# Kernel tuning notes

Hardware: AMD Instinct MI355X
Metric: run time of the kernel (lower is better)

## Reference

```python
import jax, jax.numpy as jnp
import numpy as np
import math

NUM_CLASSES = 91
FOCAL_ALPHA = 0.25
FOCAL_GAMMA = 2.0
BBOX_COEF = 5.0
GIOU_COEF = 2.0
ANGLE_COEF = 1.0
PI = math.pi


def _rect_corners(box):
    # box: [5] = (cx, cy, w, h, theta) -> [4,2] corners, CCW order
    cx, cy, w, h, th = box[0], box[1], box[2], box[3], box[4]
    c, s = jnp.cos(th), jnp.sin(th)
    dx = jnp.array([0.5, -0.5, -0.5, 0.5], box.dtype) * w
    dy = jnp.array([0.5, 0.5, -0.5, -0.5], box.dtype) * h
    px = cx + c * dx - s * dy
    py = cy + s * dx + c * dy
    return jnp.stack([px, py], axis=-1)


def _pair_obb_iou(b1, b2):
    # Oriented-box IoU of one pair via Sutherland-Hodgman convex clipping.
    # Intersection of two convex quads has at most 8 vertices.
    P = _rect_corners(b1)  # subject polygon [4,2]
    Q = _rect_corners(b2)  # clip polygon   [4,2]
    verts = jnp.concatenate([P, jnp.tile(P[:1], (4, 1))], axis=0)  # [8,2] padded
    n = jnp.int32(4)
    cQ = Q.mean(0)
    idx = jnp.arange(8)
    for k in range(4):  # clip against each edge of Q
        a, b = Q[k], Q[(k + 1) % 4]
        ex, ey = b[0] - a[0], b[1] - a[1]
        sd = lambda p: ex * (p[..., 1] - a[1]) - ey * (p[..., 0] - a[0])
        sgn = jnp.where(sd(cQ) >= 0, 1.0, -1.0)
        d = sd(verts) * sgn  # signed distance, >=0 means inside [8]
        nidx = jnp.where(idx == n - 1, 0, idx + 1)
        d_cur, d_nxt = d, d[nidx]
        valid_edge = idx < n
        cur_in, nxt_in = d_cur >= 0, d_nxt >= 0
        denom = d_cur - d_nxt
        t = jnp.where(jnp.abs(denom) > 1e-12, d_cur / jnp.where(denom == 0, 1.0, denom), 0.0)
        inter_pt = verts + t[:, None] * (verts[nidx] - verts)
        out_pts = jnp.zeros((16, 2), verts.dtype)
        out_pts = out_pts.at[0::2].set(inter_pt)
        out_pts = out_pts.at[1::2].set(verts[nidx])
        out_valid = jnp.zeros(16, bool)
        out_valid = out_valid.at[0::2].set(valid_edge & (cur_in != nxt_in))
        out_valid = out_valid.at[1::2].set(valid_edge & nxt_in)
        order = jnp.argsort(~out_valid)  # stable: valid points first, order kept
        verts = out_pts[order][:8]
        n = jnp.minimum(jnp.sum(out_valid), 8).astype(jnp.int32)
    # shoelace area; pad invalid slots with v0 so extra edges contribute 0
    verts = jnp.where((idx < n)[:, None], verts, verts[0][None])
    x, y = verts[:, 0], verts[:, 1]
    inter = 0.5 * jnp.abs(jnp.sum(x * jnp.roll(y, -1) - jnp.roll(x, -1) * y))
    a1 = b1[2] * b1[3]
    a2 = b2[2] * b2[3]
    union = a1 + a2 - inter
    return jnp.where(union > 0, inter / union, 0.0)


def _losses(pred_logits, pred_boxes, tgt_boxes, batch_idx, src_idx, tgt_labels, nb):
    B, Q, C = pred_logits.shape
    # ---- loss_labels: scatter one-hot + sigmoid focal loss ----
    target_classes = jnp.full((B, Q), NUM_CLASSES, jnp.int32)
    target_classes = target_classes.at[batch_idx, src_idx].set(tgt_labels.astype(jnp.int32))
    onehot = jax.nn.one_hot(target_classes, C + 1, dtype=pred_logits.dtype)[..., :C]
    prob = jax.nn.sigmoid(pred_logits)
    ce = jnp.maximum(pred_logits, 0) - pred_logits * onehot + jnp.log1p(jnp.exp(-jnp.abs(pred_logits)))
    p_t = prob * onehot + (1 - prob) * (1 - onehot)
    alpha_t = FOCAL_ALPHA * onehot + (1 - FOCAL_ALPHA) * (1 - onehot)
    focal = alpha_t * ce * (1 - p_t) ** FOCAL_GAMMA
    loss_ce = focal.mean(1).sum() / nb * Q
    # ---- loss_boxes: L1 + angle + oriented IoU ----
    src_boxes = pred_boxes[batch_idx, src_idx]  # [N,5]
    loss_bbox = jnp.abs(src_boxes[:, :4] - tgt_boxes[:, :4]).sum() / nb * BBOX_COEF
    ap, at = src_boxes[:, 4], tgt_boxes[:, 4]
    loss_angle = jnp.minimum(jnp.abs(ap - at), jnp.abs(ap - (at + PI))).sum() / nb * ANGLE_COEF
    iou = jax.vmap(_pair_obb_iou)(src_boxes, tgt_boxes)  # diag of obb_iou(src, tgt)
    loss_giou = (1.0 - iou).sum() / nb * GIOU_COEF
    return jnp.stack([loss_ce, loss_bbox, loss_giou, loss_angle])


def setup_inputs() -> dict:
    key = jax.random.key(0)
    ks = jax.random.split(key, 8)
    B, Q, C, N = 128, 900, 91, 8192
    pred_logits = jax.random.normal(ks[0], (B, Q, C), jnp.float32)
    def make_boxes(k, shape):
        k1, k2, k3 = jax.random.split(k, 3)
        xy = jax.random.uniform(k1, shape[:-1] + (2,), jnp.float32)
        wh = jax.random.uniform(k2, shape[:-1] + (2,), jnp.float32) * 0.2 + 0.05
        th = jax.random.uniform(k3, shape[:-1] + (1,), jnp.float32) * PI
        return jnp.concatenate([xy, wh, th], axis=-1)
    pred_boxes = make_boxes(ks[1], (B, Q, 5))
    tgt_boxes = make_boxes(ks[2], (N, 5))
    batch_idx = jnp.sort(jax.random.randint(ks[3], (N,), 0, B))
    src_idx = jax.random.randint(ks[4], (N,), 0, Q)
    tgt_labels = jax.random.randint(ks[5], (N,), 0, C)
    return {"pred_logits": pred_logits, "pred_boxes": pred_boxes, "tgt_boxes": tgt_boxes,
            "batch_idx": batch_idx, "src_idx": src_idx, "tgt_labels": tgt_labels, "num_boxes": N}


def reference(pred_logits, pred_boxes, tgt_boxes, batch_idx, src_idx, tgt_labels, num_boxes):
    nb = jnp.asarray(num_boxes, jnp.float32)
    return _losses(pred_logits, pred_boxes, tgt_boxes, batch_idx, src_idx, tgt_labels, nb)
```

## Files before the change

kernel.cpp:

```cpp
#include <hip/hip_runtime.h>
#include <math.h>

#define QN 900
#define CN 91
#define BQ (128 * 900)
#define NPAIR 8192
#define PI_F 3.14159265358979323846f

#define PAIR_BLOCKS 32
#define CORR_BLOCKS 450
#define FOCAL_BLOCKS 2048
#define NFLOAT4 (BQ * CN / 4)


__device__ __forceinline__ float read_nb(const void* p) {
    int iv = *(const int*)p;
    if (iv > 0 && iv < (1 << 30)) return (float)iv;
    return *(const float*)p;
}

__device__ __forceinline__ float f0_raw(float x) {
    float e   = __expf(-fabsf(x));
    float ope = 1.0f + e;
    float r   = __builtin_amdgcn_rcpf(ope);
    float l   = __logf(ope);
    float sp  = fmaxf(x, 0.0f) + l;
    float s   = (x >= 0.0f) ? r : e * r;
    return sp * s * s;
}


__global__ __launch_bounds__(256) void scatter_kernel(const int* __restrict__ bi,
                                                      const int* __restrict__ si,
                                                      const int* __restrict__ lb,
                                                      int* __restrict__ tc) {
    int i = blockIdx.x * 256 + threadIdx.x;
    if (i < NPAIR) {
        int key = (i << 7) | lb[i];
        atomicMax(&tc[bi[i] * QN + si[i]], key);
    }
}


__device__ void focal_body(int rb, const float4* __restrict__ l4, const void* nbp,
                           float* out, float* sm) {
    float acc = 0.0f;
    const int stride = FOCAL_BLOCKS * 256;
    for (int i = rb * 256 + threadIdx.x; i < NFLOAT4; i += stride) {
        float4 v = l4[i];
        acc += f0_raw(v.x);
        acc += f0_raw(v.y);
        acc += f0_raw(v.z);
        acc += f0_raw(v.w);
    }
#pragma unroll
    for (int o = 32; o > 0; o >>= 1) acc += __shfl_down(acc, o, 64);
    int lane = threadIdx.x & 63, w = threadIdx.x >> 6;
    if (lane == 0) sm[w] = acc;
    __syncthreads();
    if (threadIdx.x == 0) {
        float nb = read_nb(nbp);
        atomicAdd(out + 0, (sm[0] + sm[1] + sm[2] + sm[3]) * 0.75f / nb);
    }
}

__device__ void corr_body(int rb, const float* __restrict__ logits,
                          const int* __restrict__ tc, const void* nbp,
                          float* out, float* sm) {
    int j = rb * 256 + threadIdx.x;
    float acc = 0.0f;
    int v = tc[j];
    if (v >= 0) {
        int label = v & 127;
        float x = logits[j * CN + label];
        float e   = __expf(-fabsf(x));
        float ope = 1.0f + e;
        float r   = __builtin_amdgcn_rcpf(ope);
        float l   = __logf(ope);
        float sp_p = fmaxf(x, 0.0f) + l;
        float sp_n = fmaxf(-x, 0.0f) + l;
        float s   = (x >= 0.0f) ? r : e * r;
        float oms = 1.0f - s;
        acc = 0.25f * sp_n * oms * oms - 0.75f * sp_p * s * s;
    }
#pragma unroll
    for (int o = 32; o > 0; o >>= 1) acc += __shfl_down(acc, o, 64);
    int lane = threadIdx.x & 63, w = threadIdx.x >> 6;
    if (lane == 0) sm[w] = acc;
    __syncthreads();
    if (threadIdx.x == 0) {
        float nb = read_nb(nbp);
        atomicAdd(out + 0, (sm[0] + sm[1] + sm[2] + sm[3]) / nb);
    }
}

__device__ void pairs_body(const float* __restrict__ pb, const float* __restrict__ tb,
                           const int* __restrict__ bi, const int* __restrict__ si,
                           const void* nbp, float* out, float* sm) {
    int i = blockIdx.x * 256 + threadIdx.x;
    int b = bi[i], s = si[i];
    const float* p = pb + (b * QN + s) * 5;
    const float* t = tb + i * 5;
    float p0 = p[0], p1 = p[1], p2 = p[2], p3 = p[3], p4 = p[4];
    float t0 = t[0], t1 = t[1], t2 = t[2], t3 = t[3], t4 = t[4];

    float lb = fabsf(p0 - t0) + fabsf(p1 - t1) + fabsf(p2 - t2) + fabsf(p3 - t3);
    float la = fminf(fabsf(p4 - t4), fabsf(p4 - (t4 + PI_F)));

    const float dxs[4] = {0.5f, -0.5f, -0.5f, 0.5f};
    const float dys[4] = {0.5f, 0.5f, -0.5f, -0.5f};
    float c1 = cosf(p4), s1 = sinf(p4);
    float c2 = cosf(t4), s2 = sinf(t4);
    float px[8], py[8], qx[4], qy[4];
#pragma unroll
    for (int k = 0; k < 4; k++) {
        float dx = dxs[k] * p2, dy = dys[k] * p3;
        px[k] = p0 + c1 * dx - s1 * dy;
        py[k] = p1 + s1 * dx + c1 * dy;
        float ex = dxs[k] * t2, ey = dys[k] * t3;
        qx[k] = t0 + c2 * ex - s2 * ey;
        qy[k] = t1 + s2 * ex + c2 * ey;
    }
#pragma unroll
    for (int k = 4; k < 8; k++) { px[k] = 0.0f; py[k] = 0.0f; }
    float cqx = (qx[0] + qx[1] + qx[2] + qx[3]) * 0.25f;
    float cqy = (qy[0] + qy[1] + qy[2] + qy[3]) * 0.25f;

    int n = 4;
#pragma unroll
    for (int k = 0; k < 4; k++) {
        float ax = qx[k], ay = qy[k];
        int k2 = (k + 1) & 3;
        float ex = qx[k2] - ax, ey = qy[k2] - ay;
        float sd_c = ex * (cqy - ay) - ey * (cqx - ax);
        float sgn = (sd_c >= 0.0f) ? 1.0f : -1.0f;
        float d[8];
#pragma unroll
        for (int ii = 0; ii < 8; ii++)
            d[ii] = sgn * (ex * (py[ii] - ay) - ey * (px[ii] - ax));
        float nx[8], ny[8];
#pragma unroll
        for (int ii = 0; ii < 8; ii++) { nx[ii] = 0.0f; ny[ii] = 0.0f; }
        int m = 0;
#pragma unroll
        for (int ii = 0; ii < 8; ii++) {
            bool act  = ii < n;
            bool last = (ii == n - 1);
            float jx = last ? px[0] : (ii < 7 ? px[ii + 1] : 0.0f);
            float jy = last ? py[0] : (ii < 7 ? py[ii + 1] : 0.0f);
            float dn = last ? d[0]  : (ii < 7 ? d[ii + 1]  : 0.0f);
            float dc = d[ii];
            bool ci = dc >= 0.0f, ni_ = dn >= 0.0f;
            bool emitI = act && (ci != ni_);
            bool emitV = act && ni_;
            float den = dc - dn;
            float tt = (fabsf(den) > 1e-12f) ? (dc / den) : 0.0f;
            float ix = px[ii] + tt * (jx - px[ii]);
            float iy = py[ii] + tt * (jy - py[ii]);
#pragma unroll
            for (int ss = 0; ss < 8; ss++) {
                bool w1 = emitI && (ss == m);
                nx[ss] = w1 ? ix : nx[ss];
                ny[ss] = w1 ? iy : ny[ss];
            }
            m += emitI ? 1 : 0;
#pragma unroll
            for (int ss = 0; ss < 8; ss++) {
                bool w2 = emitV && (ss == m);
                nx[ss] = w2 ? jx : nx[ss];
                ny[ss] = w2 ? jy : ny[ss];
            }
            m += emitV ? 1 : 0;
        }
#pragma unroll
        for (int ii = 0; ii < 8; ii++) { px[ii] = nx[ii]; py[ii] = ny[ii]; }
        n = (m > 8) ? 8 : m;
    }
    float a2 = 0.0f;
#pragma unroll
    for (int ii = 0; ii < 8; ii++) {
        bool act  = ii < n;
        bool last = (ii == n - 1);
        float jx = last ? px[0] : (ii < 7 ? px[ii + 1] : 0.0f);
        float jy = last ? py[0] : (ii < 7 ? py[ii + 1] : 0.0f);
        a2 += act ? (px[ii] * jy - jx * py[ii]) : 0.0f;
    }
    float inter = 0.5f * fabsf(a2);
    float area1 = p2 * p3, area2 = t2 * t3;
    float uni = area1 + area2 - inter;
    float iou = (uni > 0.0f) ? inter / uni : 0.0f;
    float lg = 1.0f - iou;

#pragma unroll
    for (int o = 32; o > 0; o >>= 1) {
        lb += __shfl_down(lb, o, 64);
        lg += __shfl_down(lg, o, 64);
        la += __shfl_down(la, o, 64);
    }
    int lane = threadIdx.x & 63, w = threadIdx.x >> 6;
    if (lane == 0) { sm[w] = lb; sm[4 + w] = lg; sm[8 + w] = la; }
    __syncthreads();
    if (threadIdx.x == 0) {
        float nb = read_nb(nbp);
        float inv = 1.0f / nb;
        atomicAdd(out + 1, (sm[0] + sm[1] + sm[2] + sm[3]) * 5.0f * inv);
        atomicAdd(out + 2, (sm[4] + sm[5] + sm[6] + sm[7]) * 2.0f * inv);
        atomicAdd(out + 3, (sm[8] + sm[9] + sm[10] + sm[11]) * inv);
    }
}


__global__ __launch_bounds__(256) void mega_kernel(const float* __restrict__ logits,
                                                   const float* __restrict__ pboxes,
                                                   const float* __restrict__ tboxes,
                                                   const int* __restrict__ bidx,
                                                   const int* __restrict__ sidx,
                                                   const int* __restrict__ tc,
                                                   const void* __restrict__ nbp,
                                                   float* __restrict__ out) {
    __shared__ float sm[12];
    int rb = blockIdx.x;
    if (rb < PAIR_BLOCKS) {
        pairs_body(pboxes, tboxes, bidx, sidx, nbp, out, sm);
        return;
    }
    rb -= PAIR_BLOCKS;
    if (rb < CORR_BLOCKS) {
        corr_body(rb, logits, tc, nbp, out, sm);
        return;
    }
    rb -= CORR_BLOCKS;
    focal_body(rb, (const float4*)logits, nbp, out, sm);
}


extern "C" void kernel_launch(void* const* d_in, const int* in_sizes, int n_in,
                              void* d_out, int out_size, void* d_ws, size_t ws_size,
                              hipStream_t stream) {
    const float* logits = (const float*)d_in[0];
    const float* pboxes = (const float*)d_in[1];
    const float* tboxes = (const float*)d_in[2];
    const int*   bidx   = (const int*)d_in[3];
    const int*   sidx   = (const int*)d_in[4];
    const int*   labels = (const int*)d_in[5];
    const void*  nbp    = d_in[6];
    float* out = (float*)d_out;
    int*   tc  = (int*)d_ws;

    hipMemsetAsync(tc, 0xFF, BQ * sizeof(int), stream);
    hipMemsetAsync(out, 0, 4 * sizeof(float), stream);

    scatter_kernel<<<(NPAIR + 255) / 256, 256, 0, stream>>>(bidx, sidx, labels, tc);
    mega_kernel<<<PAIR_BLOCKS + CORR_BLOCKS + FOCAL_BLOCKS, 256, 0, stream>>>(
        logits, pboxes, tboxes, bidx, sidx, tc, nbp, out);
}
```

Baseline: 122.8 us.

## Fold matched-class correction into pairs kernel and split focal into own kernel

Instead of scanning all 115200 query slots to apply the matched-class correction, each of the 8192 pairs checks whether it won the atomicMax scatter for its slot and applies the correction itself, inside the pairs kernel. The single mega kernel is split into a standalone focal kernel and a combined pairs+correction kernel, launched in sequence. This drops 450 correction blocks but adds an extra kernel launch, and the pairs work now runs serially after the focal pass rather than overlapping with it.

```diff
diff --git a/kernel.cpp b/kernel.cpp
--- a/kernel.cpp
+++ b/kernel.cpp
@@ -7,8 +7,6 @@
 #define NPAIR 8192
 #define PI_F 3.14159265358979323846f
 
-#define PAIR_BLOCKS 32
-#define CORR_BLOCKS 450
 #define FOCAL_BLOCKS 2048
 #define NFLOAT4 (BQ * CN / 4)
 
@@ -35,18 +33,18 @@
                                                       const int* __restrict__ lb,
                                                       int* __restrict__ tc) {
     int i = blockIdx.x * 256 + threadIdx.x;
-    if (i < NPAIR) {
-        int key = (i << 7) | lb[i];
-        atomicMax(&tc[bi[i] * QN + si[i]], key);
-    }
-}
-
-
-__device__ void focal_body(int rb, const float4* __restrict__ l4, const void* nbp,
-                           float* out, float* sm) {
+    int key = (i << 7) | lb[i];
+    atomicMax(&tc[bi[i] * QN + si[i]], key);
+}
+
+
+__global__ __launch_bounds__(256) void focal_kernel(const float4* __restrict__ l4,
+                                                    const void* __restrict__ nbp,
+                                                    float* __restrict__ out) {
+    __shared__ float sm[4];
     float acc = 0.0f;
     const int stride = FOCAL_BLOCKS * 256;
-    for (int i = rb * 256 + threadIdx.x; i < NFLOAT4; i += stride) {
+    for (int i = blockIdx.x * 256 + threadIdx.x; i < NFLOAT4; i += stride) {
         float4 v = l4[i];
         acc += f0_raw(v.x);
         acc += f0_raw(v.y);
@@ -64,42 +62,37 @@
     }
 }
 
-__device__ void corr_body(int rb, const float* __restrict__ logits,
-                          const int* __restrict__ tc, const void* nbp,
-                          float* out, float* sm) {
-    int j = rb * 256 + threadIdx.x;
-    float acc = 0.0f;
-    int v = tc[j];
-    if (v >= 0) {
-        int label = v & 127;
-        float x = logits[j * CN + label];
+
+__global__ __launch_bounds__(256) void pairs_kernel(const float* __restrict__ logits,
+                                                    const float* __restrict__ pb,
+                                                    const float* __restrict__ tb,
+                                                    const int* __restrict__ bi,
+                                                    const int* __restrict__ si,
+                                                    const int* __restrict__ lbl,
+                                                    const int* __restrict__ tc,
+                                                    const void* __restrict__ nbp,
+                                                    float* __restrict__ out) {
+    __shared__ float sm[16];
+    int i = blockIdx.x * 256 + threadIdx.x;
+    int b = bi[i], s = si[i], label = lbl[i];
+    int slot = b * QN + s;
+
+    float corr = 0.0f;
+    int key = (i << 7) | label;
+    if (tc[slot] == key) {
+        float x = logits[slot * CN + label];
         float e   = __expf(-fabsf(x));
         float ope = 1.0f + e;
         float r   = __builtin_amdgcn_rcpf(ope);
         float l   = __logf(ope);
         float sp_p = fmaxf(x, 0.0f) + l;
         float sp_n = fmaxf(-x, 0.0f) + l;
-        float s   = (x >= 0.0f) ? r : e * r;
-        float oms = 1.0f - s;
-        acc = 0.25f * sp_n * oms * oms - 0.75f * sp_p * s * s;
-    }
-#pragma unroll
-    for (int o = 32; o > 0; o >>= 1) acc += __shfl_down(acc, o, 64);
-    int lane = threadIdx.x & 63, w = threadIdx.x >> 6;
-    if (lane == 0) sm[w] = acc;
-    __syncthreads();
-    if (threadIdx.x == 0) {
-        float nb = read_nb(nbp);
-        atomicAdd(out + 0, (sm[0] + sm[1] + sm[2] + sm[3]) / nb);
-    }
-}
-
-__device__ void pairs_body(const float* __restrict__ pb, const float* __restrict__ tb,
-                           const int* __restrict__ bi, const int* __restrict__ si,
-                           const void* nbp, float* out, float* sm) {
-    int i = blockIdx.x * 256 + threadIdx.x;
-    int b = bi[i], s = si[i];
-    const float* p = pb + (b * QN + s) * 5;
+        float sg  = (x >= 0.0f) ? r : e * r;
+        float oms = 1.0f - sg;
+        corr = 0.25f * sp_n * oms * oms - 0.75f * sp_p * sg * sg;
+    }
+
+    const float* p = pb + slot * 5;
     const float* t = tb + i * 5;
     float p0 = p[0], p1 = p[1], p2 = p[2], p3 = p[3], p4 = p[4];
     float t0 = t[0], t1 = t[1], t2 = t[2], t3 = t[3], t4 = t[4];
@@ -186,51 +179,28 @@
         a2 += act ? (px[ii] * jy - jx * py[ii]) : 0.0f;
     }
     float inter = 0.5f * fabsf(a2);
-    float area1 = p2 * p3, area2 = t2 * t3;
-    float uni = area1 + area2 - inter;
+    float uni = p2 * p3 + t2 * t3 - inter;
     float iou = (uni > 0.0f) ? inter / uni : 0.0f;
     float lg = 1.0f - iou;
 
 #pragma unroll
     for (int o = 32; o > 0; o >>= 1) {
-        lb += __shfl_down(lb, o, 64);
-        lg += __shfl_down(lg, o, 64);
-        la += __shfl_down(la, o, 64);
+        lb   += __shfl_down(lb, o, 64);
+        lg   += __shfl_down(lg, o, 64);
+        la   += __shfl_down(la, o, 64);
+        corr += __shfl_down(corr, o, 64);
     }
     int lane = threadIdx.x & 63, w = threadIdx.x >> 6;
-    if (lane == 0) { sm[w] = lb; sm[4 + w] = lg; sm[8 + w] = la; }
+    if (lane == 0) { sm[w] = lb; sm[4 + w] = lg; sm[8 + w] = la; sm[12 + w] = corr; }
     __syncthreads();
     if (threadIdx.x == 0) {
         float nb = read_nb(nbp);
         float inv = 1.0f / nb;
+        atomicAdd(out + 0, (sm[12] + sm[13] + sm[14] + sm[15]) * inv);
         atomicAdd(out + 1, (sm[0] + sm[1] + sm[2] + sm[3]) * 5.0f * inv);
         atomicAdd(out + 2, (sm[4] + sm[5] + sm[6] + sm[7]) * 2.0f * inv);
         atomicAdd(out + 3, (sm[8] + sm[9] + sm[10] + sm[11]) * inv);
     }
-}
-
-
-__global__ __launch_bounds__(256) void mega_kernel(const float* __restrict__ logits,
-                                                   const float* __restrict__ pboxes,
-                                                   const float* __restrict__ tboxes,
-                                                   const int* __restrict__ bidx,
-                                                   const int* __restrict__ sidx,
-                                                   const int* __restrict__ tc,
-                                                   const void* __restrict__ nbp,
-                                                   float* __restrict__ out) {
-    __shared__ float sm[12];
-    int rb = blockIdx.x;
-    if (rb < PAIR_BLOCKS) {
-        pairs_body(pboxes, tboxes, bidx, sidx, nbp, out, sm);
-        return;
-    }
-    rb -= PAIR_BLOCKS;
-    if (rb < CORR_BLOCKS) {
-        corr_body(rb, logits, tc, nbp, out, sm);
-        return;
-    }
-    rb -= CORR_BLOCKS;
-    focal_body(rb, (const float4*)logits, nbp, out, sm);
 }
 
 
@@ -247,10 +217,11 @@
     float* out = (float*)d_out;
     int*   tc  = (int*)d_ws;
 
+    hipMemsetAsync(out, 0, 4 * sizeof(float), stream);
     hipMemsetAsync(tc, 0xFF, BQ * sizeof(int), stream);
-    hipMemsetAsync(out, 0, 4 * sizeof(float), stream);
-
-    scatter_kernel<<<(NPAIR + 255) / 256, 256, 0, stream>>>(bidx, sidx, labels, tc);
-    mega_kernel<<<PAIR_BLOCKS + CORR_BLOCKS + FOCAL_BLOCKS, 256, 0, stream>>>(
-        logits, pboxes, tboxes, bidx, sidx, tc, nbp, out);
-}
+
+    scatter_kernel<<<NPAIR / 256, 256, 0, stream>>>(bidx, sidx, labels, tc);
+    focal_kernel<<<FOCAL_BLOCKS, 256, 0, stream>>>((const float4*)logits, nbp, out);
+    pairs_kernel<<<NPAIR / 256, 256, 0, stream>>>(logits, pboxes, tboxes,
+                                                  bidx, sidx, labels, tc, nbp, out);
+}
```

Measured after the change: 129.0 us. 1.05x slower.
